# Performance work log

Hardware: AMD Instinct MI355X
Metric: run time of the kernel (lower is better)

The kernel has to match this reference:

```python
import jax, jax.numpy as jnp
import numpy as np

N_ENT = 30000
ALL_REL = 221
N_DIM = 32
L = 2
EVAL_REL = 86
B = 16
E = 120000


def setup_inputs() -> dict:
    key = jax.random.key(0)
    ks = jax.random.split(key, 16)
    d = N_DIM
    inp = {
        'head': jax.random.randint(ks[0], (B,), 0, N_ENT),
        'tail': jax.random.randint(ks[1], (B,), 0, N_ENT),
        'edge_heads': jax.random.randint(ks[2], (E,), 0, N_ENT),
        'edge_tails': jax.random.randint(ks[3], (E,), 0, N_ENT),
        'edge_rels': jax.random.randint(ks[4], (E,), 0, ALL_REL),
        'edge_weight': jnp.ones((E,), jnp.float32),
        # learned params (xavier-ish scale)
        'ent_emb': jax.random.normal(ks[5], (N_ENT, d), jnp.float32) * 0.05,
        'rel_embs': jax.random.normal(ks[6], (L, ALL_REL, d), jnp.float32) * 0.1,
        'Wlin': jax.random.normal(ks[7], (L, d, d), jnp.float32) * (1.0 / np.sqrt(d)),
        'blin': jnp.zeros((L, d), jnp.float32),
        'Wrel': jax.random.normal(ks[8], (L, 2 * d, 5), jnp.float32) * 0.1,
        'brel': jnp.zeros((L, 5), jnp.float32),
        'Watt': jax.random.normal(ks[9], (L, 5, ALL_REL), jnp.float32) * 0.3,
        'batt': jnp.zeros((L, ALL_REL), jnp.float32),
        'Wr': jax.random.normal(ks[10], (4 * d, EVAL_REL), jnp.float32) * 0.1,
        'br': jnp.zeros((EVAL_REL,), jnp.float32),
    }
    return inp


def _propagate(init_emb, init_idx, ht_embed, rel_embs, Wlin, blin, Wrel, brel,
               Watt, batt, edge_weight, eh, et, er):
    # init_emb: (B, d); hiddens: (n_ent, B, d)
    Bn, d = init_emb.shape
    hid = jnp.zeros((N_ENT, Bn, d), init_emb.dtype)
    hid = hid.at[init_idx, jnp.arange(Bn)].set(init_emb)
    for l in range(L):
        # per-sample relation attention weights: (B, all_rel)
        relw = jax.nn.sigmoid(jax.nn.relu(ht_embed @ Wrel[l] + brel[l]) @ Watt[l] + batt[l])
        # generalized rspmm: out[t] += w * (relw[:, r] * rel_emb[r]) * hid[h]
        msg = hid[eh] * (relw.T[er][:, :, None] * rel_embs[l][er][:, None, :])  # (E, B, d)
        msg = msg * edge_weight[:, None, None]
        hid = jax.ops.segment_sum(msg, et, num_segments=N_ENT)  # (n_ent, B, d)
        hid = jax.nn.relu(hid @ Wlin[l] + blin[l])
    return hid


def reference(head, tail, edge_heads, edge_tails, edge_rels, edge_weight,
              ent_emb, rel_embs, Wlin, blin, Wrel, brel, Watt, batt, Wr, br):
    head_embed = ent_emb[head]  # (B, d)
    tail_embed = ent_emb[tail]
    ht_embed = jnp.concatenate([head_embed, tail_embed], axis=-1)  # (B, 2d)

    # head -> tail propagation
    hid = _propagate(head_embed, head, ht_embed, rel_embs, Wlin, blin, Wrel, brel,
                     Watt, batt, edge_weight, edge_heads, edge_tails, edge_rels)
    tail_hid = hid[tail, jnp.arange(tail.shape[0])]  # (B, d)

    # tail -> head propagation (same KG, same layers, per original code)
    hid = _propagate(tail_embed, tail, ht_embed, rel_embs, Wlin, blin, Wrel, brel,
                     Watt, batt, edge_weight, edge_heads, edge_tails, edge_rels)
    head_hid = hid[head, jnp.arange(head.shape[0])]

    embeddings = jnp.concatenate([head_embed, tail_embed, head_hid, tail_hid], axis=1)
    return embeddings @ Wr + br  # (B, eval_rel)
```

## Files before the change

### kernel.cpp

```cpp
#include <hip/hip_runtime.h>
#include <math.h>

#define N_ENTC 30000
#define ALL_RELC 221
#define NDIM 32
#define EVAL_RELC 86
#define BB 16
#define NE 120000
#define ROW 512
#define NSCAN 120
#define EPB 1000
#define MW 938


__global__ __launch_bounds__(512) void k_scan(
    const int* __restrict__ head, const int* __restrict__ tail,
    const int* __restrict__ eh, const int* __restrict__ et,
    const int* __restrict__ er, const float* __restrict__ ew,
    const float* __restrict__ ent_emb,
    const float* __restrict__ Wrel, const float* __restrict__ brel,
    const float* __restrict__ Watt, const float* __restrict__ batt,
    int4* __restrict__ recs, int* __restrict__ counts,
    float* __restrict__ relwG, float* __restrict__ hidB,
    float* __restrict__ qaccB)
{
    __shared__ unsigned mH[MW], mT[MW];
    __shared__ int s_src[32];
    __shared__ int s_cnt[4];
    __shared__ float s_ht[BB * 64];
    __shared__ float s_h5[BB * 5];
    const int t = threadIdx.x, bid = blockIdx.x;

    if (t < 32) s_src[t] = (t < BB) ? head[t] : tail[t - BB];
    for (int i = t; i < MW; i += 512) { mH[i] = 0u; mT[i] = 0u; }
    if (t < 4) s_cnt[t] = 0;
    __syncthreads();
    if (t < BB) {
        int h = s_src[t], q = s_src[BB + t];
        atomicOr(&mH[h >> 5], 1u << (h & 31));
        atomicOr(&mT[q >> 5], 1u << (q & 31));
    }
    __syncthreads();

    const int e0 = bid * EPB;
    const int4* eh4 = (const int4*)(eh + e0);
    const int4* et4 = (const int4*)(et + e0);
    for (int p = t; p < EPB / 4; p += 512) {
        int4 h4 = eh4[p], t4 = et4[p];
        int hv[4] = {h4.x, h4.y, h4.z, h4.w};
        int tv[4] = {t4.x, t4.y, t4.z, t4.w};
#pragma unroll
        for (int c = 0; c < 4; c++) {
            int e = e0 + 4 * p + c, h = hv[c], tt = tv[c];
            bool hH = (mH[h >> 5] >> (h & 31)) & 1u;
            bool hT = (mT[h >> 5] >> (h & 31)) & 1u;
            bool tT = (mT[tt >> 5] >> (tt & 31)) & 1u;
            bool tH = (mH[tt >> 5] >> (tt & 31)) & 1u;
            if (!(hH | hT | tT | tH)) continue;
            int r = er[e];
            int wb = __float_as_int(ew[e]);
            if (hH) {
                unsigned m = 0;
#pragma unroll
                for (int b = 0; b < BB; b++) m |= (s_src[b] == h) ? (1u << b) : 0u;
                int pos = atomicAdd(&s_cnt[0], 1);
                recs[(size_t)bid * EPB + pos] = make_int4(tt, r | (int)(m << 8), wb, h);
            }
            if (hT) {
                unsigned m = 0;
#pragma unroll
                for (int b = 0; b < BB; b++) m |= (s_src[BB + b] == h) ? (1u << b) : 0u;
                int pos = atomicAdd(&s_cnt[1], 1);
                recs[(size_t)NE + bid * EPB + pos] = make_int4(tt, r | (int)(m << 8), wb, h);
            }
            if (tT) {
                unsigned m = 0;
#pragma unroll
                for (int b = 0; b < BB; b++) m |= (s_src[BB + b] == tt) ? (1u << b) : 0u;
                int canon = __ffs(m) - 1;
                int pos = atomicAdd(&s_cnt[2], 1);
                recs[(size_t)2 * NE + bid * EPB + pos] = make_int4(h, r | (canon << 8), wb, tt);
            }
            if (tH) {
                unsigned m = 0;
#pragma unroll
                for (int b = 0; b < BB; b++) m |= (s_src[b] == tt) ? (1u << b) : 0u;
                int canon = __ffs(m) - 1;
                int pos = atomicAdd(&s_cnt[3], 1);
                recs[(size_t)3 * NE + bid * EPB + pos] = make_int4(h, r | (canon << 8), wb, tt);
            }
        }
    }
    __syncthreads();
    if (t < 4) counts[bid * 4 + t] = s_cnt[t];

    {
        const int wid8 = t >> 6, lane = t & 63;
        float4 z = make_float4(0.f, 0.f, 0.f, 0.f);
        for (int li = 2; li < 4; li++) {
            int c = s_cnt[li];
            float* hb = hidB + (size_t)(li - 2) * N_ENTC * ROW;
            for (int j = wid8; j < c; j += 8) {
                int row = recs[(size_t)li * NE + bid * EPB + j].x;
                float4* p = (float4*)(hb + (size_t)row * ROW);
                p[lane] = z;
                p[lane + 64] = z;
            }
        }
    }

    if (bid == 1) {
        for (int i = t; i < 2 * BB * ROW; i += 512) qaccB[i] = 0.f;
    }
    if (bid == 0) {
        for (int i = t; i < BB * NDIM; i += 512) {
            int b = i >> 5, k = i & 31;
            s_ht[b * 64 + k] = ent_emb[(size_t)s_src[b] * NDIM + k];
            s_ht[b * 64 + 32 + k] = ent_emb[(size_t)s_src[BB + b] * NDIM + k];
        }
        __syncthreads();
        for (int l = 0; l < 2; l++) {
            for (int i = t; i < BB * 5; i += 512) {
                int b = i / 5, j = i % 5;
                float s = brel[l * 5 + j];
                for (int k = 0; k < 64; k++)
                    s += s_ht[b * 64 + k] * Wrel[l * 320 + k * 5 + j];
                s_h5[i] = fmaxf(s, 0.f);
            }
            __syncthreads();
            for (int i = t; i < BB * ALL_RELC; i += 512) {
                int b = i / ALL_RELC, r = i % ALL_RELC;
                float s = batt[l * ALL_RELC + r];
                for (int j = 0; j < 5; j++)
                    s += s_h5[b * 5 + j] * Watt[l * 5 * ALL_RELC + j * ALL_RELC + r];
                relwG[l * BB * ALL_RELC + i] = 1.0f / (1.0f + expf(-s));
            }
            __syncthreads();
        }
    }
}

__global__ __launch_bounds__(256) void k_msg1(
    const int* __restrict__ head, const int* __restrict__ tail,
    const float* __restrict__ ent_emb, const float* __restrict__ rel_embs,
    const int4* __restrict__ recs, const int* __restrict__ counts,
    const float* __restrict__ relwG, float* __restrict__ hidB)
{
    __shared__ int s_src[32];
    const int t = threadIdx.x, bid = blockIdx.x;
    int4 c4 = ((const int4*)counts)[bid];
    if ((c4.x | c4.y) == 0) return;
    if (t < 32) s_src[t] = (t < BB) ? head[t] : tail[t - BB];
    __syncthreads();
    const int wid = t >> 6, lane = t & 63;
    const float4* rv0 = (const float4*)rel_embs;
    for (int d = 0; d < 2; d++) {
        int c = d ? c4.y : c4.x;
        const int4* R = recs + (size_t)d * NE + (size_t)bid * EPB;
        float* hb = hidB + (size_t)d * N_ENTC * ROW;
        for (int j = wid; j < c; j += 4) {
            int4 rec = R[j];
            int tt = rec.x, r = rec.y & 255;
            unsigned msk = ((unsigned)rec.y) >> 8;
            float w = __int_as_float(rec.z);
            float* drow = hb + (size_t)tt * ROW;
#pragma unroll
            for (int ii = 0; ii < 2; ii++) {
                int i4 = lane + 64 * ii, b = i4 >> 3, kq = i4 & 7;
                if (!((msk >> b) & 1u)) continue;
                float cf = relwG[b * ALL_RELC + r] * w;
                float4 sv = ((const float4*)(ent_emb + (size_t)s_src[d * BB + b] * NDIM))[kq];
                float4 rr = rv0[r * 8 + kq];
                atomicAdd(drow + i4 * 4 + 0, sv.x * cf * rr.x);
                atomicAdd(drow + i4 * 4 + 1, sv.y * cf * rr.y);
                atomicAdd(drow + i4 * 4 + 2, sv.z * cf * rr.z);
                atomicAdd(drow + i4 * 4 + 3, sv.w * cf * rr.w);
            }
        }
    }
}

__global__ __launch_bounds__(256) void k_lin1(
    const int4* __restrict__ recs, const int* __restrict__ counts,
    const float* __restrict__ Wlin, const float* __restrict__ blin,
    const float* __restrict__ hidB, float* __restrict__ hidC)
{
    __shared__ float sW[NDIM * NDIM];
    __shared__ float sb[NDIM];
    const int t = threadIdx.x, bid = blockIdx.x;
    int4 c4 = ((const int4*)counts)[bid];
    if ((c4.z | c4.w) == 0) return;
    for (int i = t; i < NDIM * NDIM; i += 256) sW[i] = Wlin[i];
    if (t < NDIM) sb[t] = blin[t];
    __syncthreads();
    const int wid = t >> 6, lane = t & 63;
    int b = lane >> 2, j0 = (lane & 3) * 8;
    for (int d = 0; d < 2; d++) {
        int c = d ? c4.w : c4.z;
        const int4* R = recs + (size_t)(2 + d) * NE + (size_t)bid * EPB;
        const float* hb = hidB + (size_t)d * N_ENTC * ROW;
        float* hc = hidC + (size_t)d * N_ENTC * ROW;
        for (int j = wid; j < c; j += 4) {
            int row = R[j].x;
            const float4* src = (const float4*)(hb + (size_t)row * ROW + b * NDIM);
            float h[NDIM];
#pragma unroll
            for (int q = 0; q < 8; q++) {
                float4 v = src[q];
                h[q * 4 + 0] = v.x; h[q * 4 + 1] = v.y;
                h[q * 4 + 2] = v.z; h[q * 4 + 3] = v.w;
            }
            float acc[8];
#pragma unroll
            for (int jj = 0; jj < 8; jj++) acc[jj] = sb[j0 + jj];
#pragma unroll
            for (int k = 0; k < NDIM; k++) {
                float4 w0 = *(const float4*)&sW[k * NDIM + j0];
                float4 w1 = *(const float4*)&sW[k * NDIM + j0 + 4];
                float hk = h[k];
                acc[0] += hk * w0.x; acc[1] += hk * w0.y;
                acc[2] += hk * w0.z; acc[3] += hk * w0.w;
                acc[4] += hk * w1.x; acc[5] += hk * w1.y;
                acc[6] += hk * w1.z; acc[7] += hk * w1.w;
            }
            float* dst = hc + (size_t)row * ROW + b * NDIM;
            float4 o0, o1;
            o0.x = fmaxf(acc[0], 0.f); o0.y = fmaxf(acc[1], 0.f);
            o0.z = fmaxf(acc[2], 0.f); o0.w = fmaxf(acc[3], 0.f);
            o1.x = fmaxf(acc[4], 0.f); o1.y = fmaxf(acc[5], 0.f);
            o1.z = fmaxf(acc[6], 0.f); o1.w = fmaxf(acc[7], 0.f);
            *(float4*)(dst + j0) = o0;
            *(float4*)(dst + j0 + 4) = o1;
        }
    }
}

__global__ __launch_bounds__(256) void k_msg2(
    const int4* __restrict__ recs, const int* __restrict__ counts,
    const float* __restrict__ rel_embs, const float* __restrict__ relwG,
    const float* __restrict__ hidC, float* __restrict__ qaccB)
{
    const int t = threadIdx.x, bid = blockIdx.x;
    int4 c4 = ((const int4*)counts)[bid];
    if ((c4.z | c4.w) == 0) return;
    const int wid = t >> 6, lane = t & 63;
    const float4* rv1 = (const float4*)(rel_embs + (size_t)ALL_RELC * NDIM);
    for (int d = 0; d < 2; d++) {
        int c = d ? c4.w : c4.z;
        const int4* R = recs + (size_t)(2 + d) * NE + (size_t)bid * EPB;
        const float* hc = hidC + (size_t)d * N_ENTC * ROW;
        float* qa = qaccB + (size_t)d * BB * ROW;
        for (int j = wid; j < c; j += 4) {
            int4 rec = R[j];
            int h = rec.x, r = rec.y & 255, canon = (rec.y >> 8) & 15;
            float w = __int_as_float(rec.z);
            const float4* srow = (const float4*)(hc + (size_t)h * ROW);
            float* drow = qa + canon * ROW;
#pragma unroll
            for (int ii = 0; ii < 2; ii++) {
                int i4 = lane + 64 * ii, b = i4 >> 3, kq = i4 & 7;
                float cf = relwG[BB * ALL_RELC + b * ALL_RELC + r] * w;
                float4 s = srow[i4];
                float4 rr = rv1[r * 8 + kq];
                atomicAdd(drow + i4 * 4 + 0, s.x * cf * rr.x);
                atomicAdd(drow + i4 * 4 + 1, s.y * cf * rr.y);
                atomicAdd(drow + i4 * 4 + 2, s.z * cf * rr.z);
                atomicAdd(drow + i4 * 4 + 3, s.w * cf * rr.w);
            }
        }
    }
}

__global__ __launch_bounds__(512) void k_fin(
    const int* __restrict__ head, const int* __restrict__ tail,
    const float* __restrict__ ent_emb, const float* __restrict__ Wlin,
    const float* __restrict__ blin, const float* __restrict__ Wr,
    const float* __restrict__ br, const float* __restrict__ qaccB,
    float* __restrict__ out)
{
    __shared__ float sx[BB * 128];
    __shared__ float sW[NDIM * NDIM];
    __shared__ float sb[NDIM];
    __shared__ int s_src[32];
    __shared__ int s_canon[2][BB];
    const int t = threadIdx.x;

    if (t < 32) s_src[t] = (t < BB) ? head[t] : tail[t - BB];
    for (int i = t; i < NDIM * NDIM; i += 512) sW[i] = Wlin[NDIM * NDIM + i];
    if (t < NDIM) sb[t] = blin[NDIM + t];
    __syncthreads();
    if (t < 2 * BB) {
        int d = t >> 4, b = t & 15;
        int q = s_src[(1 - d) * BB + b];
        int c = 0;
        for (int bb = 0; bb < BB; bb++)
            if (s_src[(1 - d) * BB + bb] == q) { c = bb; break; }
        s_canon[d][b] = c;
    }
    {
        int b = t >> 5, k = t & 31;
        sx[b * 128 + k] = ent_emb[(size_t)s_src[b] * NDIM + k];
        sx[b * 128 + 32 + k] = ent_emb[(size_t)s_src[BB + b] * NDIM + k];
    }
    __syncthreads();
    for (int d = 0; d < 2; d++) {
        int b = t >> 5, j = t & 31;
        const float* hrow = qaccB + (size_t)d * BB * ROW + s_canon[d][b] * ROW + b * NDIM;
        float s = sb[j];
        for (int k = 0; k < NDIM; k++)
            s += hrow[k] * sW[k * NDIM + j];
        sx[b * 128 + (d == 0 ? 96 : 64) + j] = fmaxf(s, 0.f);
    }
    __syncthreads();
    for (int o = t; o < BB * EVAL_RELC; o += 512) {
        int b = o / EVAL_RELC, r = o % EVAL_RELC;
        float s = br[r];
        for (int k = 0; k < 128; k++)
            s += sx[b * 128 + k] * Wr[k * EVAL_RELC + r];
        out[o] = s;
    }
}

extern "C" void kernel_launch(void* const* d_in, const int* in_sizes, int n_in,
                              void* d_out, int out_size, void* d_ws,
                              size_t ws_size, hipStream_t stream)
{
    const int* head = (const int*)d_in[0];
    const int* tail = (const int*)d_in[1];
    const int* eh = (const int*)d_in[2];
    const int* et = (const int*)d_in[3];
    const int* er = (const int*)d_in[4];
    const float* ew = (const float*)d_in[5];
    const float* ent_emb = (const float*)d_in[6];
    const float* rel_embs = (const float*)d_in[7];
    const float* Wlin = (const float*)d_in[8];
    const float* blin = (const float*)d_in[9];
    const float* Wrel = (const float*)d_in[10];
    const float* brel = (const float*)d_in[11];
    const float* Watt = (const float*)d_in[12];
    const float* batt = (const float*)d_in[13];
    const float* Wr = (const float*)d_in[14];
    const float* br = (const float*)d_in[15];
    float* out = (float*)d_out;
    float* ws = (float*)d_ws;

    float* hidB = ws;
    float* hidC = hidB + (size_t)2 * N_ENTC * ROW;
    int4* recs = (int4*)(hidC + (size_t)2 * N_ENTC * ROW);
    int* counts = (int*)(recs + (size_t)4 * NE);
    float* relwG = (float*)(counts + 4 * NSCAN);
    float* qaccB = relwG + 7072;

    k_scan<<<NSCAN, 512, 0, stream>>>(head, tail, eh, et, er, ew, ent_emb,
                                      Wrel, brel, Watt, batt,
                                      recs, counts, relwG, hidB, qaccB);
    k_msg1<<<NSCAN, 256, 0, stream>>>(head, tail, ent_emb, rel_embs,
                                      recs, counts, relwG, hidB);
    k_lin1<<<NSCAN, 256, 0, stream>>>(recs, counts, Wlin, blin, hidB, hidC);
    k_msg2<<<NSCAN, 256, 0, stream>>>(recs, counts, rel_embs, relwG,
                                      hidC, qaccB);
    k_fin<<<1, 512, 0, stream>>>(head, tail, ent_emb, Wlin, blin, Wr, br,
                                 qaccB, out);
}
```

Measured before the change: 121.6 us.

## Fuse all stages into one cooperative kernel and merge lin1 into msg2

Replaces the five separate kernel launches with a single cooperative kernel that uses grid-wide syncs between the scan, layer-1 message, layer-2 message and final stages. The layer-1 linear+ReLU is now computed on the fly inside the layer-2 message pass, so the hidC intermediate buffer and its writes and reads are gone. Per-block counts stay in shared memory instead of a global array. The aim is to remove launch overhead and an intermediate memory round trip. The cost is grid.sync barriers, the linear transform being recomputed for each outgoing edge rather than once per row, and the final stage running on only one block.

New measurement: 185.2 us. 52.2% more time.

```diff
diff --git a/kernel.cpp b/kernel.cpp
--- a/kernel.cpp
+++ b/kernel.cpp
@@ -1,5 +1,8 @@
 #include <hip/hip_runtime.h>
+#include <hip/hip_cooperative_groups.h>
 #include <math.h>
+
+namespace cg = cooperative_groups;
 
 #define N_ENTC 30000
 #define ALL_RELC 221
@@ -13,27 +16,36 @@
 #define MW 938
 
 
-__global__ __launch_bounds__(512) void k_scan(
+__global__ __launch_bounds__(512) void k_all(
     const int* __restrict__ head, const int* __restrict__ tail,
     const int* __restrict__ eh, const int* __restrict__ et,
     const int* __restrict__ er, const float* __restrict__ ew,
-    const float* __restrict__ ent_emb,
+    const float* __restrict__ ent_emb, const float* __restrict__ rel_embs,
+    const float* __restrict__ Wlin, const float* __restrict__ blin,
     const float* __restrict__ Wrel, const float* __restrict__ brel,
     const float* __restrict__ Watt, const float* __restrict__ batt,
-    int4* __restrict__ recs, int* __restrict__ counts,
-    float* __restrict__ relwG, float* __restrict__ hidB,
-    float* __restrict__ qaccB)
+    const float* __restrict__ Wr, const float* __restrict__ br,
+    int4* __restrict__ recs, float* __restrict__ relwG,
+    float* __restrict__ hidB, float* __restrict__ qaccB,
+    float* __restrict__ out)
 {
+    cg::grid_group grid = cg::this_grid();
     __shared__ unsigned mH[MW], mT[MW];
     __shared__ int s_src[32];
     __shared__ int s_cnt[4];
     __shared__ float s_ht[BB * 64];
     __shared__ float s_h5[BB * 5];
+    __shared__ float sW[NDIM * NDIM];
+    __shared__ float sb[NDIM];
+    __shared__ float sx[BB * 128];
+    __shared__ int s_canon[2][BB];
     const int t = threadIdx.x, bid = blockIdx.x;
 
     if (t < 32) s_src[t] = (t < BB) ? head[t] : tail[t - BB];
     for (int i = t; i < MW; i += 512) { mH[i] = 0u; mT[i] = 0u; }
     if (t < 4) s_cnt[t] = 0;
+    for (int i = t; i < NDIM * NDIM; i += 512) sW[i] = Wlin[i];
+    if (t < NDIM) sb[t] = blin[t];
     __syncthreads();
     if (t < BB) {
         int h = s_src[t], q = s_src[BB + t];
@@ -92,7 +104,6 @@
         }
     }
     __syncthreads();
-    if (t < 4) counts[bid * 4 + t] = s_cnt[t];
 
     {
         const int wid8 = t >> 6, lane = t & 63;
@@ -138,157 +149,90 @@
             __syncthreads();
         }
     }
-}
-
-__global__ __launch_bounds__(256) void k_msg1(
-    const int* __restrict__ head, const int* __restrict__ tail,
-    const float* __restrict__ ent_emb, const float* __restrict__ rel_embs,
-    const int4* __restrict__ recs, const int* __restrict__ counts,
-    const float* __restrict__ relwG, float* __restrict__ hidB)
-{
-    __shared__ int s_src[32];
-    const int t = threadIdx.x, bid = blockIdx.x;
-    int4 c4 = ((const int4*)counts)[bid];
-    if ((c4.x | c4.y) == 0) return;
-    if (t < 32) s_src[t] = (t < BB) ? head[t] : tail[t - BB];
-    __syncthreads();
-    const int wid = t >> 6, lane = t & 63;
-    const float4* rv0 = (const float4*)rel_embs;
-    for (int d = 0; d < 2; d++) {
-        int c = d ? c4.y : c4.x;
-        const int4* R = recs + (size_t)d * NE + (size_t)bid * EPB;
-        float* hb = hidB + (size_t)d * N_ENTC * ROW;
-        for (int j = wid; j < c; j += 4) {
-            int4 rec = R[j];
-            int tt = rec.x, r = rec.y & 255;
-            unsigned msk = ((unsigned)rec.y) >> 8;
-            float w = __int_as_float(rec.z);
-            float* drow = hb + (size_t)tt * ROW;
-#pragma unroll
-            for (int ii = 0; ii < 2; ii++) {
-                int i4 = lane + 64 * ii, b = i4 >> 3, kq = i4 & 7;
-                if (!((msk >> b) & 1u)) continue;
-                float cf = relwG[b * ALL_RELC + r] * w;
-                float4 sv = ((const float4*)(ent_emb + (size_t)s_src[d * BB + b] * NDIM))[kq];
-                float4 rr = rv0[r * 8 + kq];
-                atomicAdd(drow + i4 * 4 + 0, sv.x * cf * rr.x);
-                atomicAdd(drow + i4 * 4 + 1, sv.y * cf * rr.y);
-                atomicAdd(drow + i4 * 4 + 2, sv.z * cf * rr.z);
-                atomicAdd(drow + i4 * 4 + 3, sv.w * cf * rr.w);
-            }
-        }
-    }
-}
-
-__global__ __launch_bounds__(256) void k_lin1(
-    const int4* __restrict__ recs, const int* __restrict__ counts,
-    const float* __restrict__ Wlin, const float* __restrict__ blin,
-    const float* __restrict__ hidB, float* __restrict__ hidC)
-{
-    __shared__ float sW[NDIM * NDIM];
-    __shared__ float sb[NDIM];
-    const int t = threadIdx.x, bid = blockIdx.x;
-    int4 c4 = ((const int4*)counts)[bid];
-    if ((c4.z | c4.w) == 0) return;
-    for (int i = t; i < NDIM * NDIM; i += 256) sW[i] = Wlin[i];
-    if (t < NDIM) sb[t] = blin[t];
-    __syncthreads();
-    const int wid = t >> 6, lane = t & 63;
-    int b = lane >> 2, j0 = (lane & 3) * 8;
-    for (int d = 0; d < 2; d++) {
-        int c = d ? c4.w : c4.z;
-        const int4* R = recs + (size_t)(2 + d) * NE + (size_t)bid * EPB;
-        const float* hb = hidB + (size_t)d * N_ENTC * ROW;
-        float* hc = hidC + (size_t)d * N_ENTC * ROW;
-        for (int j = wid; j < c; j += 4) {
-            int row = R[j].x;
-            const float4* src = (const float4*)(hb + (size_t)row * ROW + b * NDIM);
-            float h[NDIM];
-#pragma unroll
-            for (int q = 0; q < 8; q++) {
-                float4 v = src[q];
-                h[q * 4 + 0] = v.x; h[q * 4 + 1] = v.y;
-                h[q * 4 + 2] = v.z; h[q * 4 + 3] = v.w;
-            }
-            float acc[8];
-#pragma unroll
-            for (int jj = 0; jj < 8; jj++) acc[jj] = sb[j0 + jj];
-#pragma unroll
-            for (int k = 0; k < NDIM; k++) {
-                float4 w0 = *(const float4*)&sW[k * NDIM + j0];
-                float4 w1 = *(const float4*)&sW[k * NDIM + j0 + 4];
-                float hk = h[k];
-                acc[0] += hk * w0.x; acc[1] += hk * w0.y;
-                acc[2] += hk * w0.z; acc[3] += hk * w0.w;
-                acc[4] += hk * w1.x; acc[5] += hk * w1.y;
-                acc[6] += hk * w1.z; acc[7] += hk * w1.w;
-            }
-            float* dst = hc + (size_t)row * ROW + b * NDIM;
-            float4 o0, o1;
-            o0.x = fmaxf(acc[0], 0.f); o0.y = fmaxf(acc[1], 0.f);
-            o0.z = fmaxf(acc[2], 0.f); o0.w = fmaxf(acc[3], 0.f);
-            o1.x = fmaxf(acc[4], 0.f); o1.y = fmaxf(acc[5], 0.f);
-            o1.z = fmaxf(acc[6], 0.f); o1.w = fmaxf(acc[7], 0.f);
-            *(float4*)(dst + j0) = o0;
-            *(float4*)(dst + j0 + 4) = o1;
-        }
-    }
-}
-
-__global__ __launch_bounds__(256) void k_msg2(
-    const int4* __restrict__ recs, const int* __restrict__ counts,
-    const float* __restrict__ rel_embs, const float* __restrict__ relwG,
-    const float* __restrict__ hidC, float* __restrict__ qaccB)
-{
-    const int t = threadIdx.x, bid = blockIdx.x;
-    int4 c4 = ((const int4*)counts)[bid];
-    if ((c4.z | c4.w) == 0) return;
-    const int wid = t >> 6, lane = t & 63;
-    const float4* rv1 = (const float4*)(rel_embs + (size_t)ALL_RELC * NDIM);
-    for (int d = 0; d < 2; d++) {
-        int c = d ? c4.w : c4.z;
-        const int4* R = recs + (size_t)(2 + d) * NE + (size_t)bid * EPB;
-        const float* hc = hidC + (size_t)d * N_ENTC * ROW;
-        float* qa = qaccB + (size_t)d * BB * ROW;
-        for (int j = wid; j < c; j += 4) {
-            int4 rec = R[j];
-            int h = rec.x, r = rec.y & 255, canon = (rec.y >> 8) & 15;
-            float w = __int_as_float(rec.z);
-            const float4* srow = (const float4*)(hc + (size_t)h * ROW);
-            float* drow = qa + canon * ROW;
-#pragma unroll
-            for (int ii = 0; ii < 2; ii++) {
-                int i4 = lane + 64 * ii, b = i4 >> 3, kq = i4 & 7;
-                float cf = relwG[BB * ALL_RELC + b * ALL_RELC + r] * w;
-                float4 s = srow[i4];
+
+    grid.sync();
+
+    {
+        const int wid = t >> 6, lane = t & 63;
+        const float4* rv0 = (const float4*)rel_embs;
+        for (int d = 0; d < 2; d++) {
+            int c = s_cnt[d];
+            const int4* R = recs + (size_t)d * NE + (size_t)bid * EPB;
+            float* hb = hidB + (size_t)d * N_ENTC * ROW;
+            for (int j = wid; j < c; j += 8) {
+                int4 rec = R[j];
+                int tt = rec.x, r = rec.y & 255;
+                unsigned msk = ((unsigned)rec.y) >> 8;
+                float w = __int_as_float(rec.z);
+                float* drow = hb + (size_t)tt * ROW;
+#pragma unroll
+                for (int ii = 0; ii < 2; ii++) {
+                    int i4 = lane + 64 * ii, b = i4 >> 3, kq = i4 & 7;
+                    if (!((msk >> b) & 1u)) continue;
+                    float cf = relwG[b * ALL_RELC + r] * w;
+                    float4 sv = ((const float4*)(ent_emb + (size_t)s_src[d * BB + b] * NDIM))[kq];
+                    float4 rr = rv0[r * 8 + kq];
+                    atomicAdd(drow + i4 * 4 + 0, sv.x * cf * rr.x);
+                    atomicAdd(drow + i4 * 4 + 1, sv.y * cf * rr.y);
+                    atomicAdd(drow + i4 * 4 + 2, sv.z * cf * rr.z);
+                    atomicAdd(drow + i4 * 4 + 3, sv.w * cf * rr.w);
+                }
+            }
+        }
+    }
+
+    grid.sync();
+
+    {
+        const int wid = t >> 6, lane = t & 63;
+        const int b0 = lane >> 3, kq = lane & 7, j0 = kq * 4;
+        const float4* rv1 = (const float4*)(rel_embs + (size_t)ALL_RELC * NDIM);
+        for (int d = 0; d < 2; d++) {
+            int c = s_cnt[2 + d];
+            const int4* R = recs + (size_t)(2 + d) * NE + (size_t)bid * EPB;
+            const float* hb = hidB + (size_t)d * N_ENTC * ROW;
+            float* qa = qaccB + (size_t)d * BB * ROW;
+            for (int j = wid; j < c; j += 8) {
+                int4 rec = R[j];
+                int row = rec.x, r = rec.y & 255, canon = (rec.y >> 8) & 15;
+                float w = __int_as_float(rec.z);
                 float4 rr = rv1[r * 8 + kq];
-                atomicAdd(drow + i4 * 4 + 0, s.x * cf * rr.x);
-                atomicAdd(drow + i4 * 4 + 1, s.y * cf * rr.y);
-                atomicAdd(drow + i4 * 4 + 2, s.z * cf * rr.z);
-                atomicAdd(drow + i4 * 4 + 3, s.w * cf * rr.w);
-            }
-        }
-    }
-}
-
-__global__ __launch_bounds__(512) void k_fin(
-    const int* __restrict__ head, const int* __restrict__ tail,
-    const float* __restrict__ ent_emb, const float* __restrict__ Wlin,
-    const float* __restrict__ blin, const float* __restrict__ Wr,
-    const float* __restrict__ br, const float* __restrict__ qaccB,
-    float* __restrict__ out)
-{
-    __shared__ float sx[BB * 128];
-    __shared__ float sW[NDIM * NDIM];
-    __shared__ float sb[NDIM];
-    __shared__ int s_src[32];
-    __shared__ int s_canon[2][BB];
-    const int t = threadIdx.x;
-
-    if (t < 32) s_src[t] = (t < BB) ? head[t] : tail[t - BB];
+#pragma unroll
+                for (int half = 0; half < 2; half++) {
+                    int b = b0 + 8 * half;
+                    const float4* src = (const float4*)(hb + (size_t)row * ROW + b * NDIM);
+                    float h[NDIM];
+#pragma unroll
+                    for (int q = 0; q < 8; q++) {
+                        float4 v = src[q];
+                        h[q * 4 + 0] = v.x; h[q * 4 + 1] = v.y;
+                        h[q * 4 + 2] = v.z; h[q * 4 + 3] = v.w;
+                    }
+                    float a0 = sb[j0], a1 = sb[j0 + 1], a2 = sb[j0 + 2], a3 = sb[j0 + 3];
+#pragma unroll
+                    for (int k = 0; k < NDIM; k++) {
+                        float hk = h[k];
+                        float4 wv = *(const float4*)&sW[k * NDIM + j0];
+                        a0 += hk * wv.x; a1 += hk * wv.y;
+                        a2 += hk * wv.z; a3 += hk * wv.w;
+                    }
+                    float cf = relwG[BB * ALL_RELC + b * ALL_RELC + r] * w;
+                    float* dst = qa + canon * ROW + b * NDIM + j0;
+                    atomicAdd(dst + 0, fmaxf(a0, 0.f) * cf * rr.x);
+                    atomicAdd(dst + 1, fmaxf(a1, 0.f) * cf * rr.y);
+                    atomicAdd(dst + 2, fmaxf(a2, 0.f) * cf * rr.z);
+                    atomicAdd(dst + 3, fmaxf(a3, 0.f) * cf * rr.w);
+                }
+            }
+        }
+    }
+
+    grid.sync();
+
+    if (bid != 0) return;
+
     for (int i = t; i < NDIM * NDIM; i += 512) sW[i] = Wlin[NDIM * NDIM + i];
     if (t < NDIM) sb[t] = blin[NDIM + t];
-    __syncthreads();
     if (t < 2 * BB) {
         int d = t >> 4, b = t & 15;
         int q = s_src[(1 - d) * BB + b];
@@ -345,20 +289,17 @@
     float* ws = (float*)d_ws;
 
     float* hidB = ws;
-    float* hidC = hidB + (size_t)2 * N_ENTC * ROW;
-    int4* recs = (int4*)(hidC + (size_t)2 * N_ENTC * ROW);
-    int* counts = (int*)(recs + (size_t)4 * NE);
-    float* relwG = (float*)(counts + 4 * NSCAN);
-    float* qaccB = relwG + 7072;
-
-    k_scan<<<NSCAN, 512, 0, stream>>>(head, tail, eh, et, er, ew, ent_emb,
-                                      Wrel, brel, Watt, batt,
-                                      recs, counts, relwG, hidB, qaccB);
-    k_msg1<<<NSCAN, 256, 0, stream>>>(head, tail, ent_emb, rel_embs,
-                                      recs, counts, relwG, hidB);
-    k_lin1<<<NSCAN, 256, 0, stream>>>(recs, counts, Wlin, blin, hidB, hidC);
-    k_msg2<<<NSCAN, 256, 0, stream>>>(recs, counts, rel_embs, relwG,
-                                      hidC, qaccB);
-    k_fin<<<1, 512, 0, stream>>>(head, tail, ent_emb, Wlin, blin, Wr, br,
-                                 qaccB, out);
+    int4* recs = (int4*)(hidB + (size_t)2 * N_ENTC * ROW);
+    float* relwG = (float*)(recs + (size_t)4 * NE);
+    float* qaccB = relwG + 2 * BB * ALL_RELC;
+
+    void* args[] = {
+        (void*)&head, (void*)&tail, (void*)&eh, (void*)&et, (void*)&er,
+        (void*)&ew, (void*)&ent_emb, (void*)&rel_embs, (void*)&Wlin,
+        (void*)&blin, (void*)&Wrel, (void*)&brel, (void*)&Watt, (void*)&batt,
+        (void*)&Wr, (void*)&br, (void*)&recs, (void*)&relwG, (void*)&hidB,
+        (void*)&qaccB, (void*)&out
+    };
+    hipLaunchCooperativeKernel((const void*)k_all, dim3(NSCAN), dim3(512),
+                               args, 0, stream);
 }
```
